# Optimization experiments

Measured on AMD Instinct MI355X. Metric: run time of the kernel, lower is better.

Reference implementation:

```python
import jax, jax.numpy as jnp
import numpy as np

VEC_SIZE = 256
N_VECS = 8
N_CHOICES = 2048
BATCH = 2048
EPS = 1e-6
NAND_BIAS = 3.0


def setup_inputs() -> dict:
    key = jax.random.key(0)
    k1, k2 = jax.random.split(key)
    query = jax.random.normal(k1, (BATCH, N_VECS * VEC_SIZE), dtype=jnp.float32)
    weight = jax.random.normal(k2, (N_CHOICES, VEC_SIZE * N_VECS), dtype=jnp.float32)
    # init code overwrites the randn nand_weight with ones + nand_bias
    nand_weight = jnp.full((N_CHOICES, N_VECS), 1.0 + NAND_BIAS, dtype=jnp.float32)
    return {"query": query, "weight": weight, "nand_weight": nand_weight}


def reference(query, weight, nand_weight):
    # [B, n_vecs, vec_size] and [C, n_vecs, vec_size]
    q = query.reshape(-1, N_VECS, VEC_SIZE)
    w = weight.reshape(-1, N_VECS, VEC_SIZE)
    # torch.cosine_similarity clamps each norm to eps
    qn = q / jnp.maximum(jnp.linalg.norm(q, axis=-1, keepdims=True), EPS)
    wn = w / jnp.maximum(jnp.linalg.norm(w, axis=-1, keepdims=True), EPS)
    # broadcast cosine sim expressed as batched matmul: [B, C, n_vecs]
    cos_sim = jnp.einsum('bnd,cnd->bcn', qn, wn)
    cos_sim = jax.nn.leaky_relu(cos_sim)  # slope 0.01, matches F.leaky_relu default
    nw = jax.nn.sigmoid(nand_weight)[None]  # [1, C, n_vecs]
    interpolated = nw * cos_sim + (1.0 - nw) * (1.0 - cos_sim)
    return jnp.prod(interpolated, axis=2)  # [B, C]
```

## Files before the change

### kernel.cpp

```cpp
#include <hip/hip_runtime.h>
#include <math.h>
#include <stdint.h>

#define BATCH    2048
#define NCHOICES 2048
#define NV       8
#define VS       256
#define KTOT     2048

typedef unsigned short u16;
typedef __attribute__((ext_vector_type(8))) short    bf16x8;
typedef __attribute__((ext_vector_type(8))) u16      u16x8;
typedef __attribute__((ext_vector_type(4))) float    f32x4;

__device__ __forceinline__ u16 f2bf_rne(float x) {
    unsigned u = __float_as_uint(x);
    return (u16)((u + 0x7FFFu + ((u >> 16) & 1u)) >> 16);
}

__global__ __launch_bounds__(256) void prep_convert(
    const float* __restrict__ Q, const float* __restrict__ W,
    const float* __restrict__ NWT,
    u16* __restrict__ Qh, u16* __restrict__ Ql,
    u16* __restrict__ Wh, u16* __restrict__ Wl,
    float* __restrict__ rq, float* __restrict__ rw, float* __restrict__ snw)
{
    const int row = blockIdx.x;
    const int t   = threadIdx.x;
    const int n   = t >> 5;
    const int l   = t & 31;

    const float* src; u16 *dh, *dl; float* dst;
    if (row < BATCH) {
        src = Q + (size_t)row * KTOT;
        dh = Qh + (size_t)row * KTOT; dl = Ql + (size_t)row * KTOT;
        dst = rq + (size_t)row * NV;
    } else {
        src = W + (size_t)(row - BATCH) * KTOT;
        dh = Wh + (size_t)(row - BATCH) * KTOT; dl = Wl + (size_t)(row - BATCH) * KTOT;
        dst = rw + (size_t)(row - BATCH) * NV;
    }

    const int idx = n * VS + l * 8;
    float4 x0 = *(const float4*)(src + idx);
    float4 x1 = *(const float4*)(src + idx + 4);
    float xs[8] = {x0.x, x0.y, x0.z, x0.w, x1.x, x1.y, x1.z, x1.w};

    u16x8 hv, lv;
    float s = 0.0f;
    #pragma unroll
    for (int j = 0; j < 8; ++j) {
        u16 h = f2bf_rne(xs[j]);
        float hf = __uint_as_float(((unsigned)h) << 16);
        hv[j] = h;
        lv[j] = f2bf_rne(xs[j] - hf);
        s = fmaf(xs[j], xs[j], s);
    }
    *(u16x8*)(dh + idx) = hv;
    *(u16x8*)(dl + idx) = lv;

    #pragma unroll
    for (int m = 1; m < 32; m <<= 1) s += __shfl_xor(s, m, 64);
    if (l == 0) dst[n] = 1.0f / fmaxf(sqrtf(s), 1e-6f);

    if (row >= BATCH && t < NV) {
        const int c = row - BATCH;
        float x = NWT[(size_t)c * NV + t];
        snw[(size_t)c * NV + t] = 1.0f / (1.0f + expf(-x));
    }
}

__device__ __forceinline__ void gload16(const void* g, void* l) {
    __builtin_amdgcn_global_load_lds(
        (__attribute__((address_space(1))) void*)(uintptr_t)g,
        (__attribute__((address_space(3))) void*)(uint32_t)(uintptr_t)l,
        16, 0, 0);
}

__device__ __forceinline__ bf16x8 lds_rd16(const u16* p) {
    f32x4 r;
    asm volatile("ds_read_b128 %0, %1"
                 : "=v"(r)
                 : "v"((uint32_t)(uintptr_t)p));
    return __builtin_bit_cast(bf16x8, r);
}

#define SWZ(R, G) ((R) * 32 + ((((G) ^ (((R) >> 1) & 3))) << 3))

__global__ __launch_bounds__(256, 2) void nand_mfma2b(
    const u16* __restrict__ Qh, const u16* __restrict__ Ql,
    const u16* __restrict__ Wh, const u16* __restrict__ Wl,
    const float* __restrict__ rq, const float* __restrict__ rw,
    const float* __restrict__ snw, float* __restrict__ part)
{
    __shared__ __align__(16) u16 L[2][16384];

    const int tid  = threadIdx.x;
    const int lane = tid & 63;
    const int wave = tid >> 6;
    const int wr   = (wave >> 1) * 64;
    const int wc   = (wave & 1) * 64;
    const int bm0  = blockIdx.y * 128;
    const int bn0  = blockIdx.x * 128;
    const int z    = blockIdx.z;
    const int kb   = z * 1024;

    const int fr = lane & 15;
    const int gi = lane >> 4;
    const int ri = gi * 4;

    const int lr = lane >> 2;
    const int sw = 8 * ((lane & 3) ^ ((lane >> 3) & 3));
    const int r0 = wave * 32 + lr;
    const int r1 = r0 + 16;

    const u16* sAh0 = Qh + (size_t)(bm0 + r0) * KTOT + kb + sw;
    const u16* sAh1 = Qh + (size_t)(bm0 + r1) * KTOT + kb + sw;
    const u16* sAl0 = Ql + (size_t)(bm0 + r0) * KTOT + kb + sw;
    const u16* sAl1 = Ql + (size_t)(bm0 + r1) * KTOT + kb + sw;
    const u16* sBh0 = Wh + (size_t)(bn0 + r0) * KTOT + kb + sw;
    const u16* sBh1 = Wh + (size_t)(bn0 + r1) * KTOT + kb + sw;
    const u16* sBl0 = Wl + (size_t)(bn0 + r0) * KTOT + kb + sw;
    const u16* sBl1 = Wl + (size_t)(bn0 + r1) * KTOT + kb + sw;

    #define STAGE(B, T) do { u16* Lb_ = &L[B][0]; const int ko = (T) * 32;   \
        gload16(sAh0 + ko, Lb_ + wave * 1024);                               \
        gload16(sAh1 + ko, Lb_ + wave * 1024 + 512);                         \
        gload16(sAl0 + ko, Lb_ + 4096  + wave * 1024);                       \
        gload16(sAl1 + ko, Lb_ + 4096  + wave * 1024 + 512);                 \
        gload16(sBh0 + ko, Lb_ + 8192  + wave * 1024);                       \
        gload16(sBh1 + ko, Lb_ + 8192  + wave * 1024 + 512);                 \
        gload16(sBl0 + ko, Lb_ + 12288 + wave * 1024);                       \
        gload16(sBl1 + ko, Lb_ + 12288 + wave * 1024 + 512);                 \
    } while (0)

    #define RD_A(M) do {                                                    \
        ah[M] = lds_rd16(Lb + SWZ(wr + (M) * 16 + fr, gi));                  \
        al[M] = lds_rd16(Lb + 4096 + SWZ(wr + (M) * 16 + fr, gi)); } while (0)
    #define RD_B(N) do {                                                    \
        bh[N] = lds_rd16(Lb + 8192  + SWZ(wc + (N) * 16 + fr, gi));          \
        bl[N] = lds_rd16(Lb + 12288 + SWZ(wc + (N) * 16 + fr, gi)); } while (0)

    #define MM(M, N) do {                                                   \
        acc[M][N] = __builtin_amdgcn_mfma_f32_16x16x32_bf16(ah[M], bh[N], acc[M][N], 0, 0, 0); \
        acc[M][N] = __builtin_amdgcn_mfma_f32_16x16x32_bf16(ah[M], bl[N], acc[M][N], 0, 0, 0); \
        acc[M][N] = __builtin_amdgcn_mfma_f32_16x16x32_bf16(al[M], bh[N], acc[M][N], 0, 0, 0); } while (0)

    f32x4 prod[4][4];
    #pragma unroll
    for (int m = 0; m < 4; ++m)
        #pragma unroll
        for (int n = 0; n < 4; ++n) prod[m][n] = (f32x4){1.f, 1.f, 1.f, 1.f};

    STAGE(0, 0);
    asm volatile("s_waitcnt vmcnt(0)");
    __builtin_amdgcn_s_barrier();

    int buf = 0;

    #pragma unroll 1
    for (int cc = 0; cc < 4; ++cc) {
        const int chunk = z * 4 + cc;

        f32x4 acc[4][4];
        #pragma unroll
        for (int m = 0; m < 4; ++m)
            #pragma unroll
            for (int n = 0; n < 4; ++n) acc[m][n] = (f32x4){0.f, 0.f, 0.f, 0.f};

        #pragma unroll 1
        for (int t8 = 0; t8 < 8; ++t8) {
            const int t = cc * 8 + t8;
            const u16* Lb = &L[buf][0];

            if (t + 1 < 32) STAGE(buf ^ 1, t + 1);

            bf16x8 ah[4], al[4], bh[4], bl[4];
            RD_A(0); RD_A(1); RD_A(2); RD_A(3);
            RD_B(0); RD_B(1); RD_B(2); RD_B(3);
            asm volatile("s_waitcnt lgkmcnt(0)");
            __builtin_amdgcn_sched_barrier(0);

            __builtin_amdgcn_s_setprio(1);
            MM(0, 0); MM(0, 1); MM(1, 0); MM(1, 1);
            MM(0, 2); MM(0, 3); MM(1, 2); MM(1, 3);
            MM(2, 2); MM(2, 3); MM(3, 2); MM(3, 3);
            MM(2, 0); MM(2, 1); MM(3, 0); MM(3, 1);
            __builtin_amdgcn_s_setprio(0);

            asm volatile("s_waitcnt vmcnt(0)");
            __builtin_amdgcn_s_barrier();
            buf ^= 1;
        }

        float rwv[4], vv[4], uu[4];
        #pragma unroll
        for (int n = 0; n < 4; ++n) {
            const int col = bn0 + wc + n * 16 + fr;
            rwv[n] = rw[(size_t)col * NV + chunk];
            float s = snw[(size_t)col * NV + chunk];
            vv[n] = 2.0f * s - 1.0f;
            uu[n] = 1.0f - s;
        }
        #pragma unroll
        for (int m = 0; m < 4; ++m) {
            #pragma unroll
            for (int i = 0; i < 4; ++i) {
                const float rqv =
                    rq[(size_t)(bm0 + wr + m * 16 + ri + i) * NV + chunk];
                #pragma unroll
                for (int n = 0; n < 4; ++n) {
                    float cosv = acc[m][n][i] * rqv * rwv[n];
                    float Lk = fmaxf(cosv, 0.01f * cosv);
                    prod[m][n][i] *= fmaf(Lk, vv[n], uu[n]);
                }
            }
        }
    }

    float* P = part + (size_t)z * BATCH * NCHOICES;
    #pragma unroll
    for (int m = 0; m < 4; ++m)
        #pragma unroll
        for (int i = 0; i < 4; ++i) {
            const int row = bm0 + wr + m * 16 + ri + i;
            float* pr = P + (size_t)row * NCHOICES + bn0 + wc + fr;
            #pragma unroll
            for (int n = 0; n < 4; ++n) pr[n * 16] = prod[m][n][i];
        }

    #undef STAGE
    #undef RD_A
    #undef RD_B
    #undef MM
}

__global__ __launch_bounds__(256) void combine_kernel(
    const float* __restrict__ p, float* __restrict__ out)
{
    const size_t NN = (size_t)BATCH * NCHOICES;
    size_t i = ((size_t)blockIdx.x * 256 + threadIdx.x) * 4;
    float4 a = *(const float4*)(p + i);
    float4 b = *(const float4*)(p + NN + i);
    float4 o;
    o.x = a.x * b.x;
    o.y = a.y * b.y;
    o.z = a.z * b.z;
    o.w = a.w * b.w;
    *(float4*)(out + i) = o;
}

__global__ __launch_bounds__(256) void prep_kernel(
    const float* __restrict__ Q, const float* __restrict__ W,
    const float* __restrict__ NWT,
    float* __restrict__ rq, float* __restrict__ rw, float* __restrict__ snw)
{
    const int row = blockIdx.x;
    const int t   = threadIdx.x;
    const int n   = t >> 5;
    const int l   = t & 31;

    const float* src; float* dst;
    if (row < BATCH) { src = Q + (size_t)row * KTOT; dst = rq + (size_t)row * NV; }
    else { src = W + (size_t)(row - BATCH) * KTOT; dst = rw + (size_t)(row - BATCH) * NV; }

    const float* v = src + n * VS + l * 8;
    float4 a = *(const float4*)(v);
    float4 b = *(const float4*)(v + 4);
    float s = a.x*a.x + a.y*a.y + a.z*a.z + a.w*a.w
            + b.x*b.x + b.y*b.y + b.z*b.z + b.w*b.w;
    #pragma unroll
    for (int m = 1; m < 32; m <<= 1) s += __shfl_xor(s, m, 64);
    if (l == 0) dst[n] = 1.0f / fmaxf(sqrtf(s), 1e-6f);
    if (row >= BATCH && t < NV) {
        const int c = row - BATCH;
        float x = NWT[(size_t)c * NV + t];
        snw[(size_t)c * NV + t] = 1.0f / (1.0f + expf(-x));
    }
}

__global__ __launch_bounds__(256, 2) void nand_gemm(
    const float* __restrict__ Q, const float* __restrict__ W,
    const float* __restrict__ rq, const float* __restrict__ rw,
    const float* __restrict__ snw, float* __restrict__ out)
{
    __shared__ __align__(16) float As[16][128 + 4];
    __shared__ __align__(16) float Bs[16][128 + 4];
    __shared__ __align__(16) float rqs[128];
    __shared__ __align__(16) float rws[128];
    __shared__ __align__(16) float sns[128];

    const int tid = threadIdx.x;
    const int tx  = tid & 15;
    const int ty  = tid >> 4;
    const int bm0 = blockIdx.y * 128;
    const int bn0 = blockIdx.x * 128;
    const int lr  = tid >> 2;
    const int lk  = (tid & 3) * 4;

    float prod[8][8];
    #pragma unroll
    for (int i = 0; i < 8; ++i)
        #pragma unroll
        for (int j = 0; j < 8; ++j) prod[i][j] = 1.0f;

    for (int n = 0; n < NV; ++n) {
        float acc[8][8];
        #pragma unroll
        for (int i = 0; i < 8; ++i)
            #pragma unroll
            for (int j = 0; j < 8; ++j) acc[i][j] = 0.0f;

        #pragma unroll 1
        for (int kt = 0; kt < VS / 16; ++kt) {
            const int k0 = n * VS + kt * 16;
            __syncthreads();
            {
                const float* qrow = Q + (size_t)(bm0 + lr) * KTOT + k0 + lk;
                float4 a0 = *(const float4*)(qrow);
                float4 a1 = *(const float4*)(qrow + (size_t)64 * KTOT);
                As[lk + 0][lr] = a0.x; As[lk + 1][lr] = a0.y;
                As[lk + 2][lr] = a0.z; As[lk + 3][lr] = a0.w;
                As[lk + 0][64 + lr] = a1.x; As[lk + 1][64 + lr] = a1.y;
                As[lk + 2][64 + lr] = a1.z; As[lk + 3][64 + lr] = a1.w;

                const float* wrow = W + (size_t)(bn0 + lr) * KTOT + k0 + lk;
                float4 b0 = *(const float4*)(wrow);
                float4 b1 = *(const float4*)(wrow + (size_t)64 * KTOT);
                Bs[lk + 0][lr] = b0.x; Bs[lk + 1][lr] = b0.y;
                Bs[lk + 2][lr] = b0.z; Bs[lk + 3][lr] = b0.w;
                Bs[lk + 0][64 + lr] = b1.x; Bs[lk + 1][64 + lr] = b1.y;
                Bs[lk + 2][64 + lr] = b1.z; Bs[lk + 3][64 + lr] = b1.w;
            }
            if (kt == 0) {
                for (int i = tid; i < 3 * 128; i += 256) {
                    if (i < 128)      rqs[i]       = rq[(size_t)(bm0 + i) * NV + n];
                    else if (i < 256) rws[i - 128] = rw[(size_t)(bn0 + i - 128) * NV + n];
                    else              sns[i - 256] = snw[(size_t)(bn0 + i - 256) * NV + n];
                }
            }
            __syncthreads();

            #pragma unroll
            for (int kk = 0; kk < 16; ++kk) {
                float4 a0 = *(const float4*)&As[kk][ty * 4];
                float4 a1 = *(const float4*)&As[kk][64 + ty * 4];
                float4 b0 = *(const float4*)&Bs[kk][tx * 4];
                float4 b1 = *(const float4*)&Bs[kk][64 + tx * 4];
                float ar[8] = {a0.x, a0.y, a0.z, a0.w, a1.x, a1.y, a1.z, a1.w};
                float br[8] = {b0.x, b0.y, b0.z, b0.w, b1.x, b1.y, b1.z, b1.w};
                #pragma unroll
                for (int i = 0; i < 8; ++i)
                    #pragma unroll
                    for (int j = 0; j < 8; ++j)
                        acc[i][j] = fmaf(ar[i], br[j], acc[i][j]);
            }
        }

        float rwv[8], uu[8], vv[8];
        #pragma unroll
        for (int j = 0; j < 8; ++j) {
            int cc = (j < 4) ? (tx * 4 + j) : (64 + tx * 4 + (j - 4));
            rwv[j] = rws[cc];
            float s = sns[cc];
            uu[j] = 1.0f - s;
            vv[j] = 2.0f * s - 1.0f;
        }
        #pragma unroll
        for (int i = 0; i < 8; ++i) {
            int r = (i < 4) ? (ty * 4 + i) : (64 + ty * 4 + (i - 4));
            float rqv = rqs[r];
            #pragma unroll
            for (int j = 0; j < 8; ++j) {
                float cosv = acc[i][j] * rqv * rwv[j];
                float Lk = fmaxf(cosv, 0.01f * cosv);
                prod[i][j] *= fmaf(Lk, vv[j], uu[j]);
            }
        }
    }

    #pragma unroll
    for (int i = 0; i < 8; ++i) {
        int r = (i < 4) ? (ty * 4 + i) : (64 + ty * 4 + (i - 4));
        float* orow = out + (size_t)(bm0 + r) * NCHOICES + bn0;
        float4 o0 = {prod[i][0], prod[i][1], prod[i][2], prod[i][3]};
        float4 o1 = {prod[i][4], prod[i][5], prod[i][6], prod[i][7]};
        *(float4*)(orow + tx * 4)      = o0;
        *(float4*)(orow + 64 + tx * 4) = o1;
    }
}

extern "C" void kernel_launch(void* const* d_in, const int* in_sizes, int n_in,
                              void* d_out, int out_size, void* d_ws, size_t ws_size,
                              hipStream_t stream)
{
    const float* Q   = (const float*)d_in[0];
    const float* W   = (const float*)d_in[1];
    const float* NWT = (const float*)d_in[2];
    float* out = (float*)d_out;

    char* w = (char*)d_ws;
    float* rq  = (float*)w; w += (size_t)BATCH    * NV * 4;
    float* rwn = (float*)w; w += (size_t)NCHOICES * NV * 4;
    float* snw = (float*)w; w += (size_t)NCHOICES * NV * 4;
    u16* Qh = (u16*)w; w += (size_t)BATCH * KTOT * 2;
    u16* Ql = (u16*)w; w += (size_t)BATCH * KTOT * 2;
    u16* Wh = (u16*)w; w += (size_t)NCHOICES * KTOT * 2;
    u16* Wl = (u16*)w; w += (size_t)NCHOICES * KTOT * 2;
    float* part = (float*)w; w += (size_t)2 * BATCH * NCHOICES * 4;
    const size_t needed = (size_t)(w - (char*)d_ws);

    if (ws_size >= needed) {
        prep_convert<<<BATCH + NCHOICES, 256, 0, stream>>>(
            Q, W, NWT, Qh, Ql, Wh, Wl, rq, rwn, snw);
        dim3 grid(NCHOICES / 128, BATCH / 128, 2);
        nand_mfma2b<<<grid, 256, 0, stream>>>(Qh, Ql, Wh, Wl, rq, rwn, snw, part);
        combine_kernel<<<(BATCH * NCHOICES / 4) / 256, 256, 0, stream>>>(part, out);
    } else {
        prep_kernel<<<BATCH + NCHOICES, 256, 0, stream>>>(Q, W, NWT, rq, rwn, snw);
        dim3 grid(NCHOICES / 128, BATCH / 128);
        nand_gemm<<<grid, 256, 0, stream>>>(Q, W, rq, rwn, snw, out);
    }
}
```

Measured before the change: 83.24 us.

## Overlap LDS reads with MFMAs via staged lgkmcnt waits and remap blocks

Replaces per-fragment swizzled LDS address computation with precomputed base addresses plus immediate offsets, which cuts address arithmetic. LDS reads are interleaved A/B, and MFMA groups start as soon as their operands arrive, using partial lgkmcnt waits instead of one full drain. Block indices are also remapped so consecutive launched blocks are spread in a strided order, likely to improve L2/XCD locality. The hand-counted waitcnt values must match how many loads are still in flight, and the remap changes which tiles run together.

```diff
diff --git a/kernel.cpp b/kernel.cpp
--- a/kernel.cpp
+++ b/kernel.cpp
@@ -77,15 +77,8 @@
         16, 0, 0);
 }
 
-__device__ __forceinline__ bf16x8 lds_rd16(const u16* p) {
-    f32x4 r;
-    asm volatile("ds_read_b128 %0, %1"
-                 : "=v"(r)
-                 : "v"((uint32_t)(uintptr_t)p));
-    return __builtin_bit_cast(bf16x8, r);
-}
-
-#define SWZ(R, G) ((R) * 32 + ((((G) ^ (((R) >> 1) & 3))) << 3))
+#define RD16(dst, va, OFF) \
+    asm volatile("ds_read_b128 %0, %1 offset:" OFF : "=v"(dst) : "v"(va))
 
 __global__ __launch_bounds__(256, 2) void nand_mfma2b(
     const u16* __restrict__ Qh, const u16* __restrict__ Ql,
@@ -98,11 +91,17 @@
     const int tid  = threadIdx.x;
     const int lane = tid & 63;
     const int wave = tid >> 6;
+
+    const int f    = blockIdx.x + 16 * blockIdx.y + 256 * blockIdx.z;
+    const int virt = (f & 7) * 64 + (f >> 3);
+    const int bx   = virt & 15;
+    const int by   = (virt >> 4) & 15;
+    const int z    = virt >> 8;
+
     const int wr   = (wave >> 1) * 64;
     const int wc   = (wave & 1) * 64;
-    const int bm0  = blockIdx.y * 128;
-    const int bn0  = blockIdx.x * 128;
-    const int z    = blockIdx.z;
+    const int bm0  = by * 128;
+    const int bn0  = bx * 128;
     const int kb   = z * 1024;
 
     const int fr = lane & 15;
@@ -134,12 +133,10 @@
         gload16(sBl1 + ko, Lb_ + 12288 + wave * 1024 + 512);                 \
     } while (0)
 
-    #define RD_A(M) do {                                                    \
-        ah[M] = lds_rd16(Lb + SWZ(wr + (M) * 16 + fr, gi));                  \
-        al[M] = lds_rd16(Lb + 4096 + SWZ(wr + (M) * 16 + fr, gi)); } while (0)
-    #define RD_B(N) do {                                                    \
-        bh[N] = lds_rd16(Lb + 8192  + SWZ(wc + (N) * 16 + fr, gi));          \
-        bl[N] = lds_rd16(Lb + 12288 + SWZ(wc + (N) * 16 + fr, gi)); } while (0)
+    const uint32_t ldsBase = (uint32_t)(uintptr_t)&L[0][0];
+    const uint32_t swz16   = (uint32_t)((gi ^ ((fr >> 1) & 3)) * 16);
+    const uint32_t vbaseA  = ldsBase + (uint32_t)((wr + fr) * 64) + swz16;
+    const uint32_t vbaseB  = ldsBase + 16384u + (uint32_t)((wc + fr) * 64) + swz16;
 
     #define MM(M, N) do {                                                   \
         acc[M][N] = __builtin_amdgcn_mfma_f32_16x16x32_bf16(ah[M], bh[N], acc[M][N], 0, 0, 0); \
@@ -171,21 +168,36 @@
         #pragma unroll 1
         for (int t8 = 0; t8 < 8; ++t8) {
             const int t = cc * 8 + t8;
-            const u16* Lb = &L[buf][0];
 
             if (t + 1 < 32) STAGE(buf ^ 1, t + 1);
+            __builtin_amdgcn_sched_barrier(0);
+
+            const uint32_t vaA = vbaseA + ((uint32_t)buf << 15);
+            const uint32_t vaB = vbaseB + ((uint32_t)buf << 15);
 
             bf16x8 ah[4], al[4], bh[4], bl[4];
-            RD_A(0); RD_A(1); RD_A(2); RD_A(3);
-            RD_B(0); RD_B(1); RD_B(2); RD_B(3);
+            RD16(ah[0], vaA, "0");     RD16(bh[0], vaB, "0");
+            RD16(al[0], vaA, "8192");  RD16(bl[0], vaB, "8192");
+            RD16(ah[1], vaA, "1024");  RD16(bh[1], vaB, "1024");
+            RD16(al[1], vaA, "9216");  RD16(bl[1], vaB, "9216");
+            RD16(ah[2], vaA, "2048");  RD16(bh[2], vaB, "2048");
+            RD16(al[2], vaA, "10240"); RD16(bl[2], vaB, "10240");
+            RD16(ah[3], vaA, "3072");  RD16(bh[3], vaB, "3072");
+            RD16(al[3], vaA, "11264"); RD16(bl[3], vaB, "11264");
+
+            __builtin_amdgcn_s_setprio(1);
+            asm volatile("s_waitcnt lgkmcnt(12)");
+            __builtin_amdgcn_sched_barrier(0);
+            MM(0, 0);
+            asm volatile("s_waitcnt lgkmcnt(8)");
+            __builtin_amdgcn_sched_barrier(0);
+            MM(0, 1); MM(1, 0); MM(1, 1);
+            asm volatile("s_waitcnt lgkmcnt(4)");
+            __builtin_amdgcn_sched_barrier(0);
+            MM(0, 2); MM(1, 2); MM(2, 0); MM(2, 1); MM(2, 2);
             asm volatile("s_waitcnt lgkmcnt(0)");
             __builtin_amdgcn_sched_barrier(0);
-
-            __builtin_amdgcn_s_setprio(1);
-            MM(0, 0); MM(0, 1); MM(1, 0); MM(1, 1);
-            MM(0, 2); MM(0, 3); MM(1, 2); MM(1, 3);
-            MM(2, 2); MM(2, 3); MM(3, 2); MM(3, 3);
-            MM(2, 0); MM(2, 1); MM(3, 0); MM(3, 1);
+            MM(0, 3); MM(1, 3); MM(2, 3); MM(3, 0); MM(3, 1); MM(3, 2); MM(3, 3);
             __builtin_amdgcn_s_setprio(0);
 
             asm volatile("s_waitcnt vmcnt(0)");
@@ -230,8 +242,6 @@
         }
 
     #undef STAGE
-    #undef RD_A
-    #undef RD_B
     #undef MM
 }
 
```

Result: no change. 84.41 us (+1.4%).
